# Kernel tuning notes

Hardware: AMD Instinct MI355X
Metric: run time of the kernel (lower is better)

Reference implementation:

```python
import jax, jax.numpy as jnp
from jax import lax
import numpy as np

B, T, F = 16, 1024, 128   # batch, time steps, freq bins (SPECTROGRAM_FRAME_LENGTH=1 -> frame feat = F = 128)
OUT = 61                  # phoneme classes
HID = 256


def _lengths_np():
    rng = np.random.default_rng(1)
    return rng.integers(T // 2, T + 1, size=B)


def conv2d(x, w, b, s):
    y = lax.conv_general_dilated(x, w, (s, s), 'VALID', dimension_numbers=('NCHW', 'OIHW', 'NCHW'))
    return y + b[None, :, None, None]


def bnorm(x, g, b, m, v):
    # eval-mode BatchNorm2d with running stats
    scale = g / jnp.sqrt(v + 1e-5)
    return (x - m[None, :, None, None]) * scale[None, :, None, None] + b[None, :, None, None]


def maxpool2(x):
    return lax.reduce_window(x, -np.inf, lax.max, (1, 1, 2, 2), (1, 1, 2, 2), 'VALID')


def resize_bilinear(x, h_src, H_out, W_out):
    # Bilinear resize (align_corners=False, no antialias), matching torchvision Resize on tensors.
    # x: [B,C,H,W]; per-sample valid height h_src (the crop r2[i,:,:h_i,:] is a prefix along H),
    # so gathering with indices < h_i is equivalent to resizing the cropped tensor. Vectorized over B.
    Bs, C, H, W = x.shape
    hs = h_src.astype(jnp.float32)
    c = (jnp.arange(H_out, dtype=jnp.float32)[None, :] + 0.5) * (hs[:, None] / H_out) - 0.5  # [B,H_out]
    c = jnp.maximum(c, 0.0)
    hi_max = h_src[:, None].astype(jnp.int32) - 1
    i0 = jnp.minimum(jnp.floor(c).astype(jnp.int32), hi_max)
    i1 = jnp.minimum(i0 + 1, hi_max)
    w1 = jnp.clip(c - i0.astype(jnp.float32), 0.0, 1.0)

    def gh(idx):
        return jnp.take_along_axis(x, jnp.broadcast_to(idx[:, None, :, None], (Bs, C, H_out, W)), axis=2)

    xh = gh(i0) * (1.0 - w1)[:, None, :, None] + gh(i1) * w1[:, None, :, None]  # [B,C,H_out,W]
    cw = (jnp.arange(W_out, dtype=jnp.float32) + 0.5) * (W / W_out) - 0.5
    cw = jnp.clip(cw, 0.0, W - 1.0)
    j0 = jnp.floor(cw).astype(jnp.int32)
    j1 = jnp.minimum(j0 + 1, W - 1)
    ww = cw - j0.astype(jnp.float32)
    return xh[..., j0] * (1.0 - ww) + xh[..., j1] * ww  # [B,C,H_out,W_out]


def gru_scan(x_tbd, wih, whh, bih, bhh):
    # PyTorch GRU cell, gate order (r, z, n). x_tbd: [T,B,D] -> [T,B,H]
    H = whh.shape[1]
    xW = jnp.einsum('tbd,gd->tbg', x_tbd, wih) + bih

    def step(h, xw):
        hW = h @ whh.T + bhh
        xr, xz, xn = jnp.split(xw, 3, -1)
        hr, hz, hn = jnp.split(hW, 3, -1)
        r = jax.nn.sigmoid(xr + hr)
        z = jax.nn.sigmoid(xz + hz)
        n = jnp.tanh(xn + r * hn)
        hnew = (1.0 - z) * n + z * h
        return hnew, hnew

    h0 = jnp.zeros((x_tbd.shape[1], H), x_tbd.dtype)
    return lax.scan(step, h0, xW)[1]


def bidir_gru(x, pf, pb, rev_idx):
    # x: [B,T,D]. rev_idx reverses only the valid prefix per sample (ragged lengths),
    # so the backward direction starts at each sample's true last frame, like per-sample torch GRU.
    of = gru_scan(x.transpose(1, 0, 2), *pf).transpose(1, 0, 2)
    xr = jnp.take_along_axis(x, rev_idx[:, :, None], axis=1)
    obr = gru_scan(xr.transpose(1, 0, 2), *pb).transpose(1, 0, 2)
    ob = jnp.take_along_axis(obr, rev_idx[:, :, None], axis=1)
    return jnp.concatenate([of, ob], -1)


def setup_inputs():
    keys = iter(jax.random.split(jax.random.key(0), 80))

    def rn(shape, s):
        return jax.random.normal(next(keys), shape, jnp.float32) * s

    d = {'batch': jax.random.normal(next(keys), (B, T, F), jnp.float32)}
    conv_defs = {'c1_4': (8, 1, 4), 'c1_8': (8, 1, 8), 'c1_16': (8, 1, 16), 'c1_32': (8, 1, 32),
                 'c2_4': (3, 8, 5), 'c2_8': (3, 8, 3), 'c2_16': (3, 8, 1), 'c2_32': (3, 8, 1)}
    for n, (o, i, k) in conv_defs.items():
        d[n + '_w'] = rn((o, i, k, k), 1.0 / np.sqrt(i * k * k))
        d[n + '_b'] = rn((o,), 0.05)
    for n, c in (('bn8', 8), ('bn3', 3)):
        d[n + '_g'] = 1.0 + rn((c,), 0.1)
        d[n + '_b'] = rn((c,), 0.1)
        d[n + '_m'] = rn((c,), 0.1)
        d[n + '_v'] = jax.random.uniform(next(keys), (c,), jnp.float32, 0.5, 1.5)
    d['fc1_w'] = rn((512, 5040), 0.02)
    d['fc1_b'] = rn((512,), 0.02)
    for l, din in ((0, 128 + 512), (1, 2 * HID)):
        for drc in 'fb':
            p = 'g%d%s_' % (l, drc)
            d[p + 'wih'] = rn((3 * HID, din), 1.0 / np.sqrt(HID))
            d[p + 'whh'] = rn((3 * HID, HID), 1.0 / np.sqrt(HID))
            d[p + 'bih'] = rn((3 * HID,), 0.05)
            d[p + 'bhh'] = rn((3 * HID,), 0.05)
    d['fc_w'] = rn((OUT, 2 * HID), 0.04)
    d['fc_b'] = rn((OUT,), 0.04)
    d['lengths'] = jnp.asarray(_lengths_np(), jnp.int32)
    return d


def reference(batch, c1_4_w, c1_4_b, c1_8_w, c1_8_b, c1_16_w, c1_16_b, c1_32_w, c1_32_b, c2_4_w, c2_4_b, c2_8_w, c2_8_b, c2_16_w, c2_16_b, c2_32_w, c2_32_b, bn8_g, bn8_b, bn8_m, bn8_v, bn3_g, bn3_b, bn3_m, bn3_v, fc1_w, fc1_b, g0f_wih, g0f_whh, g0f_bih, g0f_bhh, g0b_wih, g0b_whh, g0b_bih, g0b_bhh, g1f_wih, g1f_whh, g1f_bih, g1f_bhh, g1b_wih, g1b_whh, g1b_bih, g1b_bhh, fc_w, fc_b, lengths):
    Lnp = np.asarray(lengths)  # ragged lengths are static metadata
    max_len = float(Lnp.max())
    x = batch[:, None, :, :]
    # stage 1: multi-scale convs (shared bn8), relu, maxpool (dropout = identity in eval)
    r1_4 = maxpool2(jax.nn.relu(bnorm(conv2d(x, c1_4_w, c1_4_b, 1), bn8_g, bn8_b, bn8_m, bn8_v)))
    r1_8 = maxpool2(jax.nn.relu(bnorm(conv2d(x, c1_8_w, c1_8_b, 2), bn8_g, bn8_b, bn8_m, bn8_v)))
    r1_16 = maxpool2(jax.nn.relu(bnorm(conv2d(x, c1_16_w, c1_16_b, 4), bn8_g, bn8_b, bn8_m, bn8_v)))
    r1_32 = maxpool2(jax.nn.relu(bnorm(conv2d(x, c1_32_w, c1_32_b, 8), bn8_g, bn8_b, bn8_m, bn8_v)))
    # stage 2 (shared bn3)
    r2_4 = jax.nn.relu(bnorm(conv2d(r1_4, c2_4_w, c2_4_b, 3), bn3_g, bn3_b, bn3_m, bn3_v))
    r2_8 = jax.nn.relu(bnorm(conv2d(r1_8, c2_8_w, c2_8_b, 2), bn3_g, bn3_b, bn3_m, bn3_v))
    r2_16 = jax.nn.relu(bnorm(conv2d(r1_16, c2_16_w, c2_16_b, 1), bn3_g, bn3_b, bn3_m, bn3_v))
    r2_32 = jax.nn.relu(bnorm(conv2d(r1_32, c2_32_w, c2_32_b, 1), bn3_g, bn3_b, bn3_m, bn3_v))
    # per-sample crop (prefix in time) + resize to fixed sizes, fully batched
    feats = []
    for rr, (ho, wo) in ((r2_4, (90, 9)), (r2_8, (67, 6)), (r2_16, (67, 6)), (r2_32, (33, 2))):
        h_src = jnp.asarray((rr.shape[2] * (Lnp / max_len)).astype(np.int32))  # int() truncation
        feats.append(resize_bilinear(rr, h_src, ho, wo).reshape(B, -1))
    rfeat = jnp.concatenate(feats, axis=1) @ fc1_w.T + fc1_b  # [B,512]
    # frames (SPECTROGRAM_FRAME_LENGTH=1 -> frames == batch rows) + repeated global feature
    seq = jnp.concatenate([batch, jnp.broadcast_to(rfeat[:, None, :], (B, T, 512))], axis=-1)  # [B,T,640]
    tt = np.arange(T)[None, :]
    rev_idx = jnp.asarray(np.where(tt < Lnp[:, None], Lnp[:, None] - 1 - tt, tt).astype(np.int32))
    h = bidir_gru(seq, (g0f_wih, g0f_whh, g0f_bih, g0f_bhh), (g0b_wih, g0b_whh, g0b_bih, g0b_bhh), rev_idx)
    h = bidir_gru(h, (g1f_wih, g1f_whh, g1f_bih, g1f_bhh), (g1b_wih, g1b_whh, g1b_bih, g1b_bhh), rev_idx)
    preds = h @ fc_w.T + fc_b  # [B,T,OUT]
    rows = jnp.asarray(np.concatenate([i * T + np.arange(n) for i, n in enumerate(Lnp)]).astype(np.int32))
    return preds.reshape(B * T, OUT)[rows]  # [sum(lengths), OUT]
```

## Files before the change

kernel.cpp:

```cpp
#include <hip/hip_runtime.h>

typedef float f32;
typedef unsigned int u32;
typedef unsigned short u16;
typedef short s16x8 __attribute__((ext_vector_type(8)));
typedef float f32x4 __attribute__((ext_vector_type(4)));
typedef u32 u32x4 __attribute__((ext_vector_type(4)));

#define S1F (-1.4426950408889634f)
#define S2F ( 2.8853900817779268f)

__device__ __forceinline__ u16 f2bf(float x){
  u32 u = __float_as_uint(x);
  u32 r = u + 0x7FFFu + ((u >> 16) & 1u);
  return (u16)(r >> 16);
}

__global__ void k_meta(const int* __restrict__ lengths, int* __restrict__ meta){
  if (threadIdx.x == 0){
    int Lmax = 0;
    for (int b=0;b<16;b++) Lmax = max(Lmax, lengths[b]);
    meta[0] = Lmax;
    int acc = 0;
    for (int b=0;b<16;b++){ meta[1+b] = acc; acc += lengths[b]; }
    meta[17] = acc;
    const int H2s[4] = {169,126,126,62};
    for (int br=0;br<4;br++)
      for (int b=0;b<16;b++){
        double ratio = (double)lengths[b] / (double)Lmax;
        meta[32 + br*16 + b] = (int)((double)H2s[br] * ratio);
      }
  }
}

__global__ void k_wfrag(const f32* __restrict__ w0f, const f32* __restrict__ w0b,
                        const f32* __restrict__ w1f, const f32* __restrict__ w1b,
                        u16* __restrict__ wfrag){
  int idx = blockIdx.x*256 + threadIdx.x;
  int set = idx / 196608;
  int e   = idx % 196608;
  int w   = e / 24576;  int r  = e % 24576;
  int tau = r / 4096;   int r2 = r % 4096;
  int kc  = r2 >> 9;    int r3 = r2 & 511;
  int lane= r3 >> 3;    int j  = r3 & 7;
  int g = (tau>>1)*256 + w*32 + (tau&1)*16 + (lane & 15);
  int k = kc*32 + (lane>>4)*8 + j;
  const f32* src = (set==0)? w0f : (set==1)? w0b : (set==2)? w1f : w1b;
  float scale = (tau >= 4) ? S2F : S1F;
  wfrag[idx] = f2bf(src[g*256 + k] * scale);
}

__global__ void k_conv1(const f32* __restrict__ x, const f32* __restrict__ w, const f32* __restrict__ cb,
                        const f32* __restrict__ bg, const f32* __restrict__ bbp,
                        const f32* __restrict__ bm, const f32* __restrict__ bv,
                        f32* __restrict__ out, int K, int s, int Hp, int Wp){
  __shared__ f32 wl[8192];
  int b = blockIdx.y;
  int KK = K*K;
  for (int i=threadIdx.x; i<8*KK; i+=256) wl[i] = w[i];
  __syncthreads();
  int idx = blockIdx.x*256 + threadIdx.x;
  int npix = Hp*Wp;
  if (idx >= npix) return;
  int ph = idx / Wp, pw = idx % Wp;
  float mx[8];
  #pragma unroll
  for (int c=0;c<8;c++) mx[c] = -1e30f;
  for (int dy=0; dy<2; ++dy)
  for (int dx=0; dx<2; ++dx){
    const f32* xb = x + ((size_t)b*1024 + (size_t)(ph*2+dy)*s)*128 + (size_t)(pw*2+dx)*s;
    float acc[8];
    #pragma unroll
    for (int c=0;c<8;c++) acc[c] = 0.f;
    for (int kh=0; kh<K; ++kh){
      const f32* xr = xb + kh*128;
      for (int kw=0; kw<K; ++kw){
        float xv = xr[kw];
        #pragma unroll
        for (int c=0;c<8;c++) acc[c] = fmaf(xv, wl[c*KK + kh*K + kw], acc[c]);
      }
    }
    #pragma unroll
    for (int c=0;c<8;c++) mx[c] = fmaxf(mx[c], acc[c]);
  }
  #pragma unroll
  for (int c=0;c<8;c++){
    float scale = bg[c] * rsqrtf(bv[c] + 1e-5f);
    float val = (mx[c] + cb[c] - bm[c]) * scale + bbp[c];
    out[(((size_t)b*8 + c)*Hp + ph)*Wp + pw] = fmaxf(val, 0.f);
  }
}

__global__ void k_conv2(const f32* __restrict__ in, const f32* __restrict__ w, const f32* __restrict__ cb,
                        const f32* __restrict__ bg, const f32* __restrict__ bbp,
                        const f32* __restrict__ bm, const f32* __restrict__ bv,
                        f32* __restrict__ out, int K, int s, int Hin, int Win, int Ho, int Wo){
  __shared__ f32 wl[600];
  int b = blockIdx.y;
  int KK = K*K, sz = 24*KK;
  for (int i=threadIdx.x; i<sz; i+=256) wl[i] = w[i];
  __syncthreads();
  int idx = blockIdx.x*256 + threadIdx.x;
  int npix = Ho*Wo;
  if (idx >= npix) return;
  int oh = idx / Wo, ow = idx % Wo;
  float acc[3] = {0.f,0.f,0.f};
  for (int ci=0; ci<8; ++ci){
    const f32* xp = in + (((size_t)b*8 + ci)*Hin + (size_t)oh*s)*Win + (size_t)ow*s;
    for (int kh=0; kh<K; ++kh)
      for (int kw=0; kw<K; ++kw){
        float xv = xp[kh*Win + kw];
        #pragma unroll
        for (int co=0; co<3; ++co) acc[co] = fmaf(xv, wl[(co*8+ci)*KK + kh*K + kw], acc[co]);
      }
  }
  #pragma unroll
  for (int co=0; co<3; ++co){
    float scale = bg[co] * rsqrtf(bv[co] + 1e-5f);
    float val = (acc[co] + cb[co] - bm[co]) * scale + bbp[co];
    out[(((size_t)b*3 + co)*Ho + oh)*Wo + ow] = fmaxf(val, 0.f);
  }
}

__global__ void k_resize(const f32* __restrict__ src, const int* __restrict__ meta,
                         f32* __restrict__ feats, int H2, int W2, int Ho, int Wo, int off, int br){
  int idx = blockIdx.x*256 + threadIdx.x;
  int per_b = 3*Ho*Wo;
  if (idx >= 16*per_b) return;
  int b = idx / per_b;  int r = idx % per_b;
  int c = r / (Ho*Wo);  int r2 = r % (Ho*Wo);
  int ho = r2 / Wo, wo = r2 % Wo;
  int hs = meta[32 + br*16 + b];
  float cy = ((float)ho + 0.5f) * ((float)hs / (float)Ho) - 0.5f;
  cy = fmaxf(cy, 0.f);
  int him = hs - 1;
  int i0 = min((int)floorf(cy), him);
  int i1 = min(i0 + 1, him);
  float w1 = fminf(fmaxf(cy - (float)i0, 0.f), 1.f);
  float rw = (float)((double)W2 / (double)Wo);
  float cw = ((float)wo + 0.5f) * rw - 0.5f;
  cw = fminf(fmaxf(cw, 0.f), (float)(W2 - 1));
  int j0 = (int)floorf(cw);
  int j1 = min(j0 + 1, W2 - 1);
  float ww = cw - (float)j0;
  const f32* sp = src + (size_t)(b*3 + c) * H2 * W2;
  float v00 = sp[i0*W2 + j0], v01 = sp[i0*W2 + j1];
  float v10 = sp[i1*W2 + j0], v11 = sp[i1*W2 + j1];
  float col0 = v00*(1.f - w1) + v10*w1;
  float col1 = v01*(1.f - w1) + v11*w1;
  feats[(size_t)b*5040 + off + (c*Ho + ho)*Wo + wo] = col0*(1.f - ww) + col1*ww;
}

__global__ void k_fc1(const f32* __restrict__ feats, const f32* __restrict__ w,
                      const f32* __restrict__ bias, f32* __restrict__ rfeat){
  int b = blockIdx.x;
  int o0 = blockIdx.y * 64;
  int sub = threadIdx.x & 31, og = threadIdx.x >> 5;
  const f32* fp = feats + (size_t)b*5040;
  for (int oi = og; oi < 64; oi += 8){
    int o = o0 + oi;
    const f32* wp = w + (size_t)o*5040;
    float acc = 0.f;
    for (int k = sub; k < 5040; k += 32) acc = fmaf(fp[k], wp[k], acc);
    #pragma unroll
    for (int m=16; m; m>>=1) acc += __shfl_xor(acc, m, 32);
    if (sub == 0) rfeat[(size_t)b*512 + o] = acc + bias[o];
  }
}

__global__ void k_ydc(const f32* __restrict__ rfeat, const f32* __restrict__ wihf, const f32* __restrict__ wihb,
                      const f32* __restrict__ bihf, const f32* __restrict__ bihb, f32* __restrict__ ydc){
  int idx = blockIdx.x*256 + threadIdx.x;
  int d = idx / 12288;  int r = idx % 12288;
  int b = r / 768;      int g = r % 768;
  const f32* wih = d ? wihb : wihf;
  const f32* bih = d ? bihb : bihf;
  const f32* rp = rfeat + (size_t)b*512;
  const f32* wp = wih + (size_t)g*640 + 128;
  float acc = bih[g];
  for (int k=0;k<512;k++) acc = fmaf(rp[k], wp[k], acc);
  ydc[idx] = acc;
}

template<int LAYER>
__global__ __launch_bounds__(256)
void k_xw(const f32* __restrict__ A0, const f32* __restrict__ wihf, const f32* __restrict__ wihb,
          const f32* __restrict__ biasf, const f32* __restrict__ biasb,
          const f32* __restrict__ ydc, const f32* __restrict__ bhf, const f32* __restrict__ bhb,
          const int* __restrict__ lengths, f32* __restrict__ xwbuf){
  constexpr int KT   = (LAYER==0) ? 128 : 512;
  constexpr int WSTR = (LAYER==0) ? 640 : 512;
  int dir = blockIdx.z;
  const f32* wih = dir ? wihb : wihf;
  f32* out = xwbuf + (size_t)dir * 16384 * 768;
  int brow = blockIdx.x * 64, bcol = blockIdx.y * 64;
  __shared__ u32 As[1024], Bs[1024];
  int tid = threadIdx.x, lane = tid & 63, wid = tid >> 6;
  int rl = tid >> 2, kg = tid & 3;
  int grow = brow + rl;
  int tt = grow >> 4, bb = grow & 15;
  int srct = tt;
  if (dir){ int L = lengths[bb]; srct = (tt < L) ? (L - 1 - tt) : tt; }
  const f32* arow = A0 + ((size_t)bb*1024 + srct) * KT;
  const f32* brp  = wih + (size_t)(bcol + rl) * WSTR;
  int swst = kg ^ ((rl >> 1) & 3);
  u32* adst = &As[rl*16 + swst*4];
  u32* bdst = &Bs[rl*16 + swst*4];
  int r16 = wid*16 + (lane & 15);
  int grp = lane >> 4;
  int aoff = r16*16 + ((grp ^ ((r16 >> 1) & 3)) * 4);
  f32x4 acc[4];
  #pragma unroll
  for (int nt=0; nt<4; ++nt) acc[nt] = (f32x4){0.f,0.f,0.f,0.f};

  for (int kc=0; kc<KT/32; ++kc){
    int k0 = kc*32 + kg*8;
    {
      f32x4 av0 = *(const f32x4*)(arow + k0);
      f32x4 av1 = *(const f32x4*)(arow + k0 + 4);
      u32 p0 = (u32)f2bf(av0[0]) | ((u32)f2bf(av0[1])<<16);
      u32 p1 = (u32)f2bf(av0[2]) | ((u32)f2bf(av0[3])<<16);
      u32 p2 = (u32)f2bf(av1[0]) | ((u32)f2bf(av1[1])<<16);
      u32 p3 = (u32)f2bf(av1[2]) | ((u32)f2bf(av1[3])<<16);
      u32x4 v = {p0,p1,p2,p3};
      *(u32x4*)adst = v;
      f32x4 bv0 = *(const f32x4*)(brp + k0);
      f32x4 bv1 = *(const f32x4*)(brp + k0 + 4);
      u32 q0 = (u32)f2bf(bv0[0]) | ((u32)f2bf(bv0[1])<<16);
      u32 q1 = (u32)f2bf(bv0[2]) | ((u32)f2bf(bv0[3])<<16);
      u32 q2 = (u32)f2bf(bv1[0]) | ((u32)f2bf(bv1[1])<<16);
      u32 q3 = (u32)f2bf(bv1[2]) | ((u32)f2bf(bv1[3])<<16);
      u32x4 u = {q0,q1,q2,q3};
      *(u32x4*)bdst = u;
    }
    __syncthreads();
    s16x8 a = *(const s16x8*)&As[aoff];
    #pragma unroll
    for (int nt=0; nt<4; ++nt){
      int gl = nt*16 + (lane & 15);
      s16x8 bfr = *(const s16x8*)&Bs[gl*16 + ((grp ^ ((gl >> 1) & 3)) * 4)];
      acc[nt] = __builtin_amdgcn_mfma_f32_16x16x32_bf16(a, bfr, acc[nt], 0, 0, 0);
    }
    __syncthreads();
  }
  const f32* bh = dir ? bhb : bhf;
  #pragma unroll
  for (int nt=0; nt<4; ++nt){
    int col = bcol + nt*16 + (lane & 15);
    float bhadd = (col < 512) ? bh[col] : 0.f;
    float scale = (col < 512) ? S1F : S2F;
    #pragma unroll
    for (int q=0; q<4; ++q){
      int row = brow + wid*16 + (lane >> 4)*4 + q;
      float bias;
      if (LAYER == 0) bias = ydc[((size_t)dir*16 + (row & 15))*768 + col];
      else            bias = (dir ? biasb : biasf)[col];
      out[(size_t)row*768 + col] = (acc[nt][q] + bias + bhadd) * scale;
    }
  }
}

#define GRU_STEP(t_, u_, X_) do { \
  f32x4 a_r0={0.f,0.f,0.f,0.f}, a_r1={0.f,0.f,0.f,0.f}; \
  f32x4 a_z0={0.f,0.f,0.f,0.f}, a_z1={0.f,0.f,0.f,0.f}; \
  f32x4 a_n0={bhn0,bhn0,bhn0,bhn0}, a_n1={bhn1,bhn1,bhn1,bhn1}; \
  _Pragma("unroll") \
  for (int kc=0; kc<8; ++kc){ \
    s16x8 a = *(const s16x8*)&h_lds[(u_)*576 + hro + kc*32 + lq*8]; \
    a_r0 = __builtin_amdgcn_mfma_f32_16x16x32_bf16(a, wreg[0][kc], a_r0, 0,0,0); \
    a_r1 = __builtin_amdgcn_mfma_f32_16x16x32_bf16(a, wreg[1][kc], a_r1, 0,0,0); \
    a_z0 = __builtin_amdgcn_mfma_f32_16x16x32_bf16(a, wreg[2][kc], a_z0, 0,0,0); \
    a_z1 = __builtin_amdgcn_mfma_f32_16x16x32_bf16(a, wreg[3][kc], a_z1, 0,0,0); \
    a_n0 = __builtin_amdgcn_mfma_f32_16x16x32_bf16(a, wreg[4][kc], a_n0, 0,0,0); \
    a_n1 = __builtin_amdgcn_mfma_f32_16x16x32_bf16(a, wreg[5][kc], a_n1, 0,0,0); \
  } \
  { \
    float ar0 = qi ? a_r0[1] : a_r0[0], ar1 = qi ? a_r1[1] : a_r1[0]; \
    float az0 = qi ? a_z0[1] : a_z0[0], az1 = qi ? a_z1[1] : a_z1[0]; \
    float an0 = qi ? a_n0[1] : a_n0[0], an1 = qi ? a_n1[1] : a_n1[0]; \
    float ar = tpi ? ar1 : ar0; \
    float az = tpi ? az1 : az0; \
    float an = tpi ? an1 : an0; \
    float r = __builtin_amdgcn_rcpf(1.0f + __builtin_amdgcn_exp2f(X_[0] + ar)); \
    float z = __builtin_amdgcn_rcpf(1.0f + __builtin_amdgcn_exp2f(X_[1] + az)); \
    float n = fmaf(-2.0f, __builtin_amdgcn_rcpf(__builtin_amdgcn_exp2f(fmaf(r, an, X_[2])) + 1.0f), 1.0f); \
    float hv = fmaf(z, hp - n, n); \
    hp = hv; \
    u32 ub = __float_as_uint(hv); \
    h_lds[((u_)^1)*576 + qi*288 + jme] = (u16)((ub + 0x8000u)>>16); \
    if (dir == 0){ *hpt = hv; hpt += 512; } \
    else { int tpos = ((t_) < Lq) ? (Lq-1-(t_)) : (t_); hpt[(size_t)tpos*512] = hv; } \
  } \
  asm volatile("s_waitcnt lgkmcnt(0)\n\ts_barrier" ::: "memory"); \
} while(0)

template<int LAYER>
__global__ __launch_bounds__(512, 2)
void k_recur(const f32* __restrict__ xw, const u16* __restrict__ wfrag,
             const f32* __restrict__ bhhf, const f32* __restrict__ bhhb,
             const int* __restrict__ lengths, f32* __restrict__ hout){
  __shared__ u16 h_lds[1152];
  const int dir = blockIdx.y;
  const int b0  = blockIdx.x * 2;
  const int tid = threadIdx.x, lane = tid & 63, wid = tid >> 6;
  const f32* xwd = xw + (size_t)dir * 12582912;
  const f32* bhh = dir ? bhhb : bhhf;
  const u16* wf = wfrag + (size_t)(LAYER*2 + dir) * 196608;

  s16x8 wreg[6][8];
  #pragma unroll
  for (int tau=0; tau<6; ++tau)
    #pragma unroll
    for (int kc=0; kc<8; ++kc)
      wreg[tau][kc] = *(const s16x8*)(wf + ((size_t)((wid*6+tau)*8 + kc)*64 + lane)*8);
  if (tid < 576) ((u32*)h_lds)[tid] = 0;

  const int l15 = lane & 15, lq = lane >> 4;
  const int jlo = (wid << 5) + l15;
  const int hro = (l15 & 1) * 288;
  const int qi  = lq & 1;
  const int tpi = lq >> 1;
  const int jme = jlo + tpi*16;
  const float bhn0 = bhh[512 + jlo] * S2F;
  const float bhn1 = bhh[512 + jlo + 16] * S2F;
  const int Lq = lengths[b0 + qi];
  float hp = 0.f;

  const f32* xp = xwd + (size_t)(b0+qi)*768 + jme;
  f32* hpt = hout + (size_t)(b0+qi)*1024*512 + dir*256 + jme;

  float X0[3], X1[3];
  X0[0]=xp[0]; X0[1]=xp[256]; X0[2]=xp[512]; xp += 12288;
  X1[0]=xp[0]; X1[1]=xp[256]; X1[2]=xp[512]; xp += 12288;
  __syncthreads();

  for (int t2=0; t2<1024; t2+=2){
    GRU_STEP(t2,   0, X0);
    X0[0]=xp[0]; X0[1]=xp[256]; X0[2]=xp[512]; xp += 12288;
    GRU_STEP(t2+1, 1, X1);
    X1[0]=xp[0]; X1[1]=xp[256]; X1[2]=xp[512]; xp += 12288;
  }
}

__global__ void k_final(const f32* __restrict__ h1, const f32* __restrict__ fcw, const f32* __restrict__ fcb,
                        const int* __restrict__ lengths, const int* __restrict__ meta, f32* __restrict__ out){
  int t = blockIdx.x, b = blockIdx.y;
  if (t >= lengths[b]) return;
  __shared__ f32 part[4][64];
  int lane = threadIdx.x & 63, q = threadIdx.x >> 6;
  float acc = 0.f;
  if (lane < 61){
    const f32* wp = fcw + (size_t)lane*512 + q*128;
    const f32* hp = h1 + ((size_t)b*1024 + t)*512 + q*128;
    for (int k=0;k<128;k++) acc = fmaf(hp[k], wp[k], acc);
  }
  part[q][lane] = acc;
  __syncthreads();
  if (q == 0 && lane < 61){
    int row = meta[1 + b] + t;
    out[(size_t)row*61 + lane] = part[0][lane] + part[1][lane] + part[2][lane] + part[3][lane] + fcb[lane];
  }
}

extern "C" void kernel_launch(void* const* d_in, const int* in_sizes, int n_in,
                              void* d_out, int out_size, void* d_ws, size_t ws_size,
                              hipStream_t stream){
  const f32* batch = (const f32*)d_in[0];
  const f32* c1w[4] = {(const f32*)d_in[1],(const f32*)d_in[3],(const f32*)d_in[5],(const f32*)d_in[7]};
  const f32* c1b[4] = {(const f32*)d_in[2],(const f32*)d_in[4],(const f32*)d_in[6],(const f32*)d_in[8]};
  const f32* c2w[4] = {(const f32*)d_in[9],(const f32*)d_in[11],(const f32*)d_in[13],(const f32*)d_in[15]};
  const f32* c2b[4] = {(const f32*)d_in[10],(const f32*)d_in[12],(const f32*)d_in[14],(const f32*)d_in[16]};
  const f32 *bn8g=(const f32*)d_in[17], *bn8b=(const f32*)d_in[18], *bn8m=(const f32*)d_in[19], *bn8v=(const f32*)d_in[20];
  const f32 *bn3g=(const f32*)d_in[21], *bn3b=(const f32*)d_in[22], *bn3m=(const f32*)d_in[23], *bn3v=(const f32*)d_in[24];
  const f32 *fc1w=(const f32*)d_in[25], *fc1b=(const f32*)d_in[26];
  const f32 *g0f_wih=(const f32*)d_in[27], *g0f_whh=(const f32*)d_in[28], *g0f_bih=(const f32*)d_in[29], *g0f_bhh=(const f32*)d_in[30];
  const f32 *g0b_wih=(const f32*)d_in[31], *g0b_whh=(const f32*)d_in[32], *g0b_bih=(const f32*)d_in[33], *g0b_bhh=(const f32*)d_in[34];
  const f32 *g1f_wih=(const f32*)d_in[35], *g1f_whh=(const f32*)d_in[36], *g1f_bih=(const f32*)d_in[37], *g1f_bhh=(const f32*)d_in[38];
  const f32 *g1b_wih=(const f32*)d_in[39], *g1b_whh=(const f32*)d_in[40], *g1b_bih=(const f32*)d_in[41], *g1b_bhh=(const f32*)d_in[42];
  const f32 *fcw=(const f32*)d_in[43], *fcb=(const f32*)d_in[44];
  const int* lengths = (const int*)d_in[45];
  f32* out = (f32*)d_out;

  char* base = (char*)d_ws;
  size_t off = 0;
  auto alloc = [&](size_t bytes)->void*{
    void* p = base + off;
    off += bytes;
    off = (off + 255) & ~(size_t)255;
    return p;
  };

  static const int Hp[4]={510,254,126,62}, Wpp[4]={62,30,14,6};
  static const int K1[4]={4,8,16,32}, S1[4]={1,2,4,8};
  static const int K2[4]={5,3,1,1},  S2[4]={3,2,1,1};
  static const int Ho2[4]={169,126,126,62}, Wo2[4]={20,14,14,6};
  static const int Hr[4]={90,67,67,33}, Wr[4]={9,6,6,2};
  static const int Foff[4]={0,2430,3636,4842};

  f32* r1[4]; for (int i=0;i<4;i++) r1[i] = (f32*)alloc((size_t)16*8*Hp[i]*Wpp[i]*4);
  f32* r2[4]; for (int i=0;i<4;i++) r2[i] = (f32*)alloc((size_t)16*3*Ho2[i]*Wo2[i]*4);
  f32* feats = (f32*)alloc((size_t)16*5040*4);
  f32* rfeat = (f32*)alloc((size_t)16*512*4);
  f32* ydc   = (f32*)alloc((size_t)2*16*768*4);
  int* meta  = (int*)alloc(128*4);
  u16* wfrag = (u16*)alloc((size_t)4*196608*2);
  f32* xwb   = (f32*)alloc((size_t)2*1024*16*768*4);
  f32* h0    = (f32*)alloc((size_t)16*1024*512*4);
  f32* h1p   = (f32*)alloc((size_t)16*1024*512*4);

  k_meta<<<1,64,0,stream>>>(lengths, meta);
  k_wfrag<<<3072,256,0,stream>>>(g0f_whh, g0b_whh, g1f_whh, g1b_whh, wfrag);
  for (int i=0;i<4;i++){
    int np = Hp[i]*Wpp[i];
    k_conv1<<<dim3((np+255)/256,16),256,0,stream>>>(batch, c1w[i], c1b[i], bn8g,bn8b,bn8m,bn8v,
                                                    r1[i], K1[i], S1[i], Hp[i], Wpp[i]);
  }
  for (int i=0;i<4;i++){
    int np = Ho2[i]*Wo2[i];
    k_conv2<<<dim3((np+255)/256,16),256,0,stream>>>(r1[i], c2w[i], c2b[i], bn3g,bn3b,bn3m,bn3v,
                                                    r2[i], K2[i], S2[i], Hp[i], Wpp[i], Ho2[i], Wo2[i]);
  }
  for (int i=0;i<4;i++){
    int tot = 16*3*Hr[i]*Wr[i];
    k_resize<<<(tot+255)/256,256,0,stream>>>(r2[i], meta, feats, Ho2[i], Wo2[i], Hr[i], Wr[i], Foff[i], i);
  }
  k_fc1<<<dim3(16,8),256,0,stream>>>(feats, fc1w, fc1b, rfeat);
  k_ydc<<<96,256,0,stream>>>(rfeat, g0f_wih, g0b_wih, g0f_bih, g0b_bih, ydc);
  k_xw<0><<<dim3(256,12,2),256,0,stream>>>(batch, g0f_wih, g0b_wih, nullptr, nullptr, ydc, g0f_bhh, g0b_bhh, lengths, xwb);
  k_recur<0><<<dim3(8,2),512,0,stream>>>(xwb, wfrag, g0f_bhh, g0b_bhh, lengths, h0);
  k_xw<1><<<dim3(256,12,2),256,0,stream>>>(h0, g1f_wih, g1b_wih, g1f_bih, g1b_bih, nullptr, g1f_bhh, g1b_bhh, lengths, xwb);
  k_recur<1><<<dim3(8,2),512,0,stream>>>(xwb, wfrag, g1f_bhh, g1b_bhh, lengths, h1p);
  k_final<<<dim3(1024,16),256,0,stream>>>(h1p, fcw, fcb, lengths, meta, out);
}
```

Baseline: 2.914 ms.

## Store hidden states in bf16, pre-convert GEMM operands, merge branch launches

Several changes at once. Input and Wih weights are converted to bf16 once in a merged prep kernel, and k_xw loads them straight into LDS with global_load_lds instead of converting in the loop. The recurrence now writes bf16 hidden states, which halves the h buffer traffic. The per-branch conv and resize launches are merged into single grid-z kernels, and k_final is restructured to process 16 timesteps per block with vectorized loads. The extra bf16 rounding of h now also feeds the final FC, which may slightly change numerics.

```diff
diff --git a/kernel.cpp b/kernel.cpp
--- a/kernel.cpp
+++ b/kernel.cpp
@@ -16,8 +16,48 @@
   return (u16)(r >> 16);
 }
 
-__global__ void k_meta(const int* __restrict__ lengths, int* __restrict__ meta){
-  if (threadIdx.x == 0){
+__device__ __forceinline__ void gld16(const u16* g, u16* l){
+  __builtin_amdgcn_global_load_lds((const __attribute__((address_space(1))) u32*)g,
+                                   (__attribute__((address_space(3))) u32*)l, 16, 0, 0);
+}
+
+__global__ void k_prep(const f32* __restrict__ w0f, const f32* __restrict__ w0b,
+                       const f32* __restrict__ w1f, const f32* __restrict__ w1b,
+                       const f32* __restrict__ wih0f, const f32* __restrict__ wih0b,
+                       const f32* __restrict__ wih1f, const f32* __restrict__ wih1b,
+                       const f32* __restrict__ batch, const int* __restrict__ lengths,
+                       u16* __restrict__ wfrag, u16* __restrict__ wihbf,
+                       u16* __restrict__ batchbf, int* __restrict__ meta){
+  const int bx = blockIdx.x, tid = threadIdx.x;
+  if (bx < 3072){
+    int idx = bx*256 + tid;
+    int set = idx / 196608;
+    int e   = idx % 196608;
+    int w   = e / 24576;  int r  = e % 24576;
+    int tau = r / 4096;   int r2 = r % 4096;
+    int kc  = r2 >> 9;    int r3 = r2 & 511;
+    int lane= r3 >> 3;    int j  = r3 & 7;
+    int g = (tau>>1)*256 + w*32 + (tau&1)*16 + (lane & 15);
+    int k = kc*32 + (lane>>4)*8 + j;
+    const f32* src = (set==0)? w0f : (set==1)? w0b : (set==2)? w1f : w1b;
+    float scale = (tau >= 4) ? S2F : S1F;
+    wfrag[idx] = f2bf(src[g*256 + k] * scale);
+  } else if (bx < 6912){
+    int idx = (bx-3072)*256 + tid;
+    if (idx < 196608){
+      int d = idx / 98304; int r = idx % 98304;
+      int g = r >> 7, k = r & 127;
+      wihbf[idx] = f2bf((d ? wih0b : wih0f)[g*640 + k]);
+    } else {
+      int i2 = idx - 196608;
+      int d = i2 / 393216; int r = i2 % 393216;
+      int g = r >> 9, k = r & 511;
+      wihbf[idx] = f2bf((d ? wih1b : wih1f)[g*512 + k]);
+    }
+  } else if (bx < 15104){
+    int idx = (bx-6912)*256 + tid;
+    batchbf[idx] = f2bf(batch[idx]);
+  } else if (tid == 0){
     int Lmax = 0;
     for (int b=0;b<16;b++) Lmax = max(Lmax, lengths[b]);
     meta[0] = Lmax;
@@ -33,27 +73,18 @@
   }
 }
 
-__global__ void k_wfrag(const f32* __restrict__ w0f, const f32* __restrict__ w0b,
-                        const f32* __restrict__ w1f, const f32* __restrict__ w1b,
-                        u16* __restrict__ wfrag){
-  int idx = blockIdx.x*256 + threadIdx.x;
-  int set = idx / 196608;
-  int e   = idx % 196608;
-  int w   = e / 24576;  int r  = e % 24576;
-  int tau = r / 4096;   int r2 = r % 4096;
-  int kc  = r2 >> 9;    int r3 = r2 & 511;
-  int lane= r3 >> 3;    int j  = r3 & 7;
-  int g = (tau>>1)*256 + w*32 + (tau&1)*16 + (lane & 15);
-  int k = kc*32 + (lane>>4)*8 + j;
-  const f32* src = (set==0)? w0f : (set==1)? w0b : (set==2)? w1f : w1b;
-  float scale = (tau >= 4) ? S2F : S1F;
-  wfrag[idx] = f2bf(src[g*256 + k] * scale);
-}
-
-__global__ void k_conv1(const f32* __restrict__ x, const f32* __restrict__ w, const f32* __restrict__ cb,
-                        const f32* __restrict__ bg, const f32* __restrict__ bbp,
-                        const f32* __restrict__ bm, const f32* __restrict__ bv,
-                        f32* __restrict__ out, int K, int s, int Hp, int Wp){
+__global__ void k_conv1a(const f32* __restrict__ x,
+                         const f32* __restrict__ w0,const f32* __restrict__ w1,const f32* __restrict__ w2,const f32* __restrict__ w3,
+                         const f32* __restrict__ cb0,const f32* __restrict__ cb1,const f32* __restrict__ cb2,const f32* __restrict__ cb3,
+                         const f32* __restrict__ bg, const f32* __restrict__ bbp,
+                         const f32* __restrict__ bm, const f32* __restrict__ bv,
+                         f32* __restrict__ o0, f32* __restrict__ o1, f32* __restrict__ o2, f32* __restrict__ o3){
+  const int br = blockIdx.z;
+  const int Ks[4]={4,8,16,32}, Ss[4]={1,2,4,8}, Hps[4]={510,254,126,62}, Wps[4]={62,30,14,6};
+  const int K = Ks[br], s = Ss[br], Hp = Hps[br], Wp = Wps[br];
+  const f32* w  = (br==0)?w0:(br==1)?w1:(br==2)?w2:w3;
+  const f32* cb = (br==0)?cb0:(br==1)?cb1:(br==2)?cb2:cb3;
+  f32* out      = (br==0)?o0:(br==1)?o1:(br==2)?o2:o3;
   __shared__ f32 wl[8192];
   int b = blockIdx.y;
   int KK = K*K;
@@ -91,10 +122,20 @@
   }
 }
 
-__global__ void k_conv2(const f32* __restrict__ in, const f32* __restrict__ w, const f32* __restrict__ cb,
-                        const f32* __restrict__ bg, const f32* __restrict__ bbp,
-                        const f32* __restrict__ bm, const f32* __restrict__ bv,
-                        f32* __restrict__ out, int K, int s, int Hin, int Win, int Ho, int Wo){
+__global__ void k_conv2a(const f32* __restrict__ i0,const f32* __restrict__ i1,const f32* __restrict__ i2,const f32* __restrict__ i3,
+                         const f32* __restrict__ w0,const f32* __restrict__ w1,const f32* __restrict__ w2,const f32* __restrict__ w3,
+                         const f32* __restrict__ cb0,const f32* __restrict__ cb1,const f32* __restrict__ cb2,const f32* __restrict__ cb3,
+                         const f32* __restrict__ bg, const f32* __restrict__ bbp,
+                         const f32* __restrict__ bm, const f32* __restrict__ bv,
+                         f32* __restrict__ o0, f32* __restrict__ o1, f32* __restrict__ o2, f32* __restrict__ o3){
+  const int br = blockIdx.z;
+  const int Ks[4]={5,3,1,1}, Ss[4]={3,2,1,1}, Hins[4]={510,254,126,62}, Wins[4]={62,30,14,6};
+  const int Hos[4]={169,126,126,62}, Wos[4]={20,14,14,6};
+  const int K = Ks[br], s = Ss[br], Hin = Hins[br], Win = Wins[br], Ho = Hos[br], Wo = Wos[br];
+  const f32* in = (br==0)?i0:(br==1)?i1:(br==2)?i2:i3;
+  const f32* w  = (br==0)?w0:(br==1)?w1:(br==2)?w2:w3;
+  const f32* cb = (br==0)?cb0:(br==1)?cb1:(br==2)?cb2:cb3;
+  f32* out      = (br==0)?o0:(br==1)?o1:(br==2)?o2:o3;
   __shared__ f32 wl[600];
   int b = blockIdx.y;
   int KK = K*K, sz = 24*KK;
@@ -122,8 +163,13 @@
   }
 }
 
-__global__ void k_resize(const f32* __restrict__ src, const int* __restrict__ meta,
-                         f32* __restrict__ feats, int H2, int W2, int Ho, int Wo, int off, int br){
+__global__ void k_resizea(const f32* __restrict__ s0,const f32* __restrict__ s1,const f32* __restrict__ s2,const f32* __restrict__ s3,
+                          const int* __restrict__ meta, f32* __restrict__ feats){
+  const int br = blockIdx.z;
+  const int H2s[4]={169,126,126,62}, W2s[4]={20,14,14,6}, Hos[4]={90,67,67,33}, Wos[4]={9,6,6,2};
+  const int offs[4]={0,2430,3636,4842};
+  const int H2 = H2s[br], W2 = W2s[br], Ho = Hos[br], Wo = Wos[br], off = offs[br];
+  const f32* src = (br==0)?s0:(br==1)?s1:(br==2)?s2:s3;
   int idx = blockIdx.x*256 + threadIdx.x;
   int per_b = 3*Ho*Wo;
   if (idx >= 16*per_b) return;
@@ -175,70 +221,55 @@
   int b = r / 768;      int g = r % 768;
   const f32* wih = d ? wihb : wihf;
   const f32* bih = d ? bihb : bihf;
-  const f32* rp = rfeat + (size_t)b*512;
-  const f32* wp = wih + (size_t)g*640 + 128;
+  const f32x4* rp = (const f32x4*)(rfeat + (size_t)b*512);
+  const f32x4* wp = (const f32x4*)(wih + (size_t)g*640 + 128);
   float acc = bih[g];
-  for (int k=0;k<512;k++) acc = fmaf(rp[k], wp[k], acc);
+  for (int k=0;k<128;k++){
+    f32x4 a = rp[k], w4 = wp[k];
+    acc = fmaf(a[0],w4[0],acc); acc = fmaf(a[1],w4[1],acc);
+    acc = fmaf(a[2],w4[2],acc); acc = fmaf(a[3],w4[3],acc);
+  }
   ydc[idx] = acc;
 }
 
 template<int LAYER>
 __global__ __launch_bounds__(256)
-void k_xw(const f32* __restrict__ A0, const f32* __restrict__ wihf, const f32* __restrict__ wihb,
+void k_xw(const u16* __restrict__ Abf, const u16* __restrict__ wihbf,
           const f32* __restrict__ biasf, const f32* __restrict__ biasb,
           const f32* __restrict__ ydc, const f32* __restrict__ bhf, const f32* __restrict__ bhb,
           const int* __restrict__ lengths, f32* __restrict__ xwbuf){
-  constexpr int KT   = (LAYER==0) ? 128 : 512;
-  constexpr int WSTR = (LAYER==0) ? 640 : 512;
-  int dir = blockIdx.z;
-  const f32* wih = dir ? wihb : wihf;
+  constexpr int KT = (LAYER==0) ? 128 : 512;
+  const int dir = blockIdx.z;
   f32* out = xwbuf + (size_t)dir * 16384 * 768;
-  int brow = blockIdx.x * 64, bcol = blockIdx.y * 64;
-  __shared__ u32 As[1024], Bs[1024];
-  int tid = threadIdx.x, lane = tid & 63, wid = tid >> 6;
-  int rl = tid >> 2, kg = tid & 3;
-  int grow = brow + rl;
-  int tt = grow >> 4, bb = grow & 15;
+  const u16* wd = wihbf + (size_t)dir * 768 * KT;
+  const int brow = blockIdx.x * 64, bcol = blockIdx.y * 64;
+  __shared__ __attribute__((aligned(16))) u16 As[2048], Bs[2048];
+  const int tid = threadIdx.x, lane = tid & 63, wid = tid >> 6;
+  const int srow = wid*16 + (lane >> 2);
+  const int cg   = (lane & 3) ^ (srow & 3);
+  int tt = (brow + srow) >> 4, bb = (brow + srow) & 15;
   int srct = tt;
   if (dir){ int L = lengths[bb]; srct = (tt < L) ? (L - 1 - tt) : tt; }
-  const f32* arow = A0 + ((size_t)bb*1024 + srct) * KT;
-  const f32* brp  = wih + (size_t)(bcol + rl) * WSTR;
-  int swst = kg ^ ((rl >> 1) & 3);
-  u32* adst = &As[rl*16 + swst*4];
-  u32* bdst = &Bs[rl*16 + swst*4];
-  int r16 = wid*16 + (lane & 15);
-  int grp = lane >> 4;
-  int aoff = r16*16 + ((grp ^ ((r16 >> 1) & 3)) * 4);
+  const u16* asrc = Abf + ((size_t)bb*1024 + srct)*KT + cg*8;
+  const u16* bsrc = wd + (size_t)(bcol + srow)*KT + cg*8;
+  u16* adst = As + wid*512;
+  u16* bdst = Bs + wid*512;
+  const int l15 = lane & 15, grp = lane >> 4;
+  const int arow_f = wid*16 + l15;
+  const int aoff = arow_f*32 + ((grp ^ (arow_f & 3))*8);
   f32x4 acc[4];
   #pragma unroll
   for (int nt=0; nt<4; ++nt) acc[nt] = (f32x4){0.f,0.f,0.f,0.f};
 
   for (int kc=0; kc<KT/32; ++kc){
-    int k0 = kc*32 + kg*8;
-    {
-      f32x4 av0 = *(const f32x4*)(arow + k0);
-      f32x4 av1 = *(const f32x4*)(arow + k0 + 4);
-      u32 p0 = (u32)f2bf(av0[0]) | ((u32)f2bf(av0[1])<<16);
-      u32 p1 = (u32)f2bf(av0[2]) | ((u32)f2bf(av0[3])<<16);
-      u32 p2 = (u32)f2bf(av1[0]) | ((u32)f2bf(av1[1])<<16);
-      u32 p3 = (u32)f2bf(av1[2]) | ((u32)f2bf(av1[3])<<16);
-      u32x4 v = {p0,p1,p2,p3};
-      *(u32x4*)adst = v;
-      f32x4 bv0 = *(const f32x4*)(brp + k0);
-      f32x4 bv1 = *(const f32x4*)(brp + k0 + 4);
-      u32 q0 = (u32)f2bf(bv0[0]) | ((u32)f2bf(bv0[1])<<16);
-      u32 q1 = (u32)f2bf(bv0[2]) | ((u32)f2bf(bv0[3])<<16);
-      u32 q2 = (u32)f2bf(bv1[0]) | ((u32)f2bf(bv1[1])<<16);
-      u32 q3 = (u32)f2bf(bv1[2]) | ((u32)f2bf(bv1[3])<<16);
-      u32x4 u = {q0,q1,q2,q3};
-      *(u32x4*)bdst = u;
-    }
+    gld16(asrc + kc*32, adst);
+    gld16(bsrc + kc*32, bdst);
     __syncthreads();
     s16x8 a = *(const s16x8*)&As[aoff];
     #pragma unroll
     for (int nt=0; nt<4; ++nt){
-      int gl = nt*16 + (lane & 15);
-      s16x8 bfr = *(const s16x8*)&Bs[gl*16 + ((grp ^ ((gl >> 1) & 3)) * 4)];
+      int cb = nt*16 + l15;
+      s16x8 bfr = *(const s16x8*)&Bs[cb*32 + ((grp ^ (cb & 3))*8)];
       acc[nt] = __builtin_amdgcn_mfma_f32_16x16x32_bf16(a, bfr, acc[nt], 0, 0, 0);
     }
     __syncthreads();
@@ -246,12 +277,12 @@
   const f32* bh = dir ? bhb : bhf;
   #pragma unroll
   for (int nt=0; nt<4; ++nt){
-    int col = bcol + nt*16 + (lane & 15);
+    int col = bcol + nt*16 + l15;
     float bhadd = (col < 512) ? bh[col] : 0.f;
     float scale = (col < 512) ? S1F : S2F;
     #pragma unroll
     for (int q=0; q<4; ++q){
-      int row = brow + wid*16 + (lane >> 4)*4 + q;
+      int row = brow + wid*16 + grp*4 + q;
       float bias;
       if (LAYER == 0) bias = ydc[((size_t)dir*16 + (row & 15))*768 + col];
       else            bias = (dir ? biasb : biasf)[col];
@@ -287,9 +318,10 @@
     float hv = fmaf(z, hp - n, n); \
     hp = hv; \
     u32 ub = __float_as_uint(hv); \
-    h_lds[((u_)^1)*576 + qi*288 + jme] = (u16)((ub + 0x8000u)>>16); \
-    if (dir == 0){ *hpt = hv; hpt += 512; } \
-    else { int tpos = ((t_) < Lq) ? (Lq-1-(t_)) : (t_); hpt[(size_t)tpos*512] = hv; } \
+    u16 hb16 = (u16)((ub + 0x8000u)>>16); \
+    h_lds[((u_)^1)*576 + qi*288 + jme] = hb16; \
+    if (dir == 0){ *hb = hb16; hb += 512; } \
+    else { int tpos = ((t_) < Lq) ? (Lq-1-(t_)) : (t_); hb[(size_t)tpos*512] = hb16; } \
   } \
   asm volatile("s_waitcnt lgkmcnt(0)\n\ts_barrier" ::: "memory"); \
 } while(0)
@@ -298,7 +330,7 @@
 __global__ __launch_bounds__(512, 2)
 void k_recur(const f32* __restrict__ xw, const u16* __restrict__ wfrag,
              const f32* __restrict__ bhhf, const f32* __restrict__ bhhb,
-             const int* __restrict__ lengths, f32* __restrict__ hout){
+             const int* __restrict__ lengths, u16* __restrict__ hbf){
   __shared__ u16 h_lds[1152];
   const int dir = blockIdx.y;
   const int b0  = blockIdx.x * 2;
@@ -327,7 +359,7 @@
   float hp = 0.f;
 
   const f32* xp = xwd + (size_t)(b0+qi)*768 + jme;
-  f32* hpt = hout + (size_t)(b0+qi)*1024*512 + dir*256 + jme;
+  u16* hb = hbf + ((size_t)(b0+qi)*1024)*512 + dir*256 + jme;
 
   float X0[3], X1[3];
   X0[0]=xp[0]; X0[1]=xp[256]; X0[2]=xp[512]; xp += 12288;
@@ -342,23 +374,37 @@
   }
 }
 
-__global__ void k_final(const f32* __restrict__ h1, const f32* __restrict__ fcw, const f32* __restrict__ fcb,
+__global__ void k_final(const u16* __restrict__ h1, const f32* __restrict__ fcw, const f32* __restrict__ fcb,
                         const int* __restrict__ lengths, const int* __restrict__ meta, f32* __restrict__ out){
-  int t = blockIdx.x, b = blockIdx.y;
-  if (t >= lengths[b]) return;
-  __shared__ f32 part[4][64];
-  int lane = threadIdx.x & 63, q = threadIdx.x >> 6;
-  float acc = 0.f;
-  if (lane < 61){
-    const f32* wp = fcw + (size_t)lane*512 + q*128;
-    const f32* hp = h1 + ((size_t)b*1024 + t)*512 + q*128;
-    for (int k=0;k<128;k++) acc = fmaf(hp[k], wp[k], acc);
-  }
-  part[q][lane] = acc;
-  __syncthreads();
-  if (q == 0 && lane < 61){
-    int row = meta[1 + b] + t;
-    out[(size_t)row*61 + lane] = part[0][lane] + part[1][lane] + part[2][lane] + part[3][lane] + fcb[lane];
+  int b = blockIdx.y;
+  int t0 = blockIdx.x * 16;
+  int lane = threadIdx.x & 63, w = threadIdx.x >> 6;
+  int L = lengths[b];
+  if (t0 >= L) return;
+  const f32* wp = fcw + (size_t)lane*512;
+  float bias = (lane < 61) ? fcb[lane] : 0.f;
+  int rowbase = meta[1 + b];
+  #pragma unroll
+  for (int p=0;p<4;p++){
+    int t = t0 + p*4 + w;
+    if (t < L && lane < 61){
+      const u16* hp = h1 + ((size_t)b*1024 + t)*512;
+      float acc = 0.f;
+      for (int k8=0;k8<64;k8++){
+        u32x4 hv = *(const u32x4*)(hp + k8*8);
+        f32x4 w0 = *(const f32x4*)(wp + k8*8);
+        f32x4 w1 = *(const f32x4*)(wp + k8*8 + 4);
+        acc = fmaf(__uint_as_float(hv[0] << 16),        w0[0], acc);
+        acc = fmaf(__uint_as_float(hv[0] & 0xffff0000u),w0[1], acc);
+        acc = fmaf(__uint_as_float(hv[1] << 16),        w0[2], acc);
+        acc = fmaf(__uint_as_float(hv[1] & 0xffff0000u),w0[3], acc);
+        acc = fmaf(__uint_as_float(hv[2] << 16),        w1[0], acc);
+        acc = fmaf(__uint_as_float(hv[2] & 0xffff0000u),w1[1], acc);
+        acc = fmaf(__uint_as_float(hv[3] << 16),        w1[2], acc);
+        acc = fmaf(__uint_as_float(hv[3] & 0xffff0000u),w1[3], acc);
+      }
+      out[(size_t)(rowbase + t)*61 + lane] = acc + bias;
+    }
   }
 }
 
@@ -391,11 +437,7 @@
   };
 
   static const int Hp[4]={510,254,126,62}, Wpp[4]={62,30,14,6};
-  static const int K1[4]={4,8,16,32}, S1[4]={1,2,4,8};
-  static const int K2[4]={5,3,1,1},  S2[4]={3,2,1,1};
   static const int Ho2[4]={169,126,126,62}, Wo2[4]={20,14,14,6};
-  static const int Hr[4]={90,67,67,33}, Wr[4]={9,6,6,2};
-  static const int Foff[4]={0,2430,3636,4842};
 
   f32* r1[4]; for (int i=0;i<4;i++) r1[i] = (f32*)alloc((size_t)16*8*Hp[i]*Wpp[i]*4);
   f32* r2[4]; for (int i=0;i<4;i++) r2[i] = (f32*)alloc((size_t)16*3*Ho2[i]*Wo2[i]*4);
@@ -404,31 +446,30 @@
   f32* ydc   = (f32*)alloc((size_t)2*16*768*4);
   int* meta  = (int*)alloc(128*4);
   u16* wfrag = (u16*)alloc((size_t)4*196608*2);
+  u16* wihbf = (u16*)alloc((size_t)983040*2);
+  u16* batchbf=(u16*)alloc((size_t)16*1024*128*2);
   f32* xwb   = (f32*)alloc((size_t)2*1024*16*768*4);
-  f32* h0    = (f32*)alloc((size_t)16*1024*512*4);
-  f32* h1p   = (f32*)alloc((size_t)16*1024*512*4);
-
-  k_meta<<<1,64,0,stream>>>(lengths, meta);
-  k_wfrag<<<3072,256,0,stream>>>(g0f_whh, g0b_whh, g1f_whh, g1b_whh, wfrag);
-  for (int i=0;i<4;i++){
-    int np = Hp[i]*Wpp[i];
-    k_conv1<<<dim3((np+255)/256,16),256,0,stream>>>(batch, c1w[i], c1b[i], bn8g,bn8b,bn8m,bn8v,
-                                                    r1[i], K1[i], S1[i], Hp[i], Wpp[i]);
-  }
-  for (int i=0;i<4;i++){
-    int np = Ho2[i]*Wo2[i];
-    k_conv2<<<dim3((np+255)/256,16),256,0,stream>>>(r1[i], c2w[i], c2b[i], bn3g,bn3b,bn3m,bn3v,
-                                                    r2[i], K2[i], S2[i], Hp[i], Wpp[i], Ho2[i], Wo2[i]);
-  }
-  for (int i=0;i<4;i++){
-    int tot = 16*3*Hr[i]*Wr[i];
-    k_resize<<<(tot+255)/256,256,0,stream>>>(r2[i], meta, feats, Ho2[i], Wo2[i], Hr[i], Wr[i], Foff[i], i);
-  }
+  u16* hbf0  = (u16*)alloc((size_t)16*1024*512*2);
+  u16* hbf1  = (u16*)alloc((size_t)16*1024*512*2);
+
+  k_prep<<<15105,256,0,stream>>>(g0f_whh, g0b_whh, g1f_whh, g1b_whh,
+                                 g0f_wih, g0b_wih, g1f_wih, g1b_wih,
+                                 batch, lengths, wfrag, wihbf, batchbf, meta);
+  k_conv1a<<<dim3(124,16,4),256,0,stream>>>(batch, c1w[0],c1w[1],c1w[2],c1w[3],
+                                            c1b[0],c1b[1],c1b[2],c1b[3],
+                                            bn8g,bn8b,bn8m,bn8v, r1[0],r1[1],r1[2],r1[3]);
+  k_conv2a<<<dim3(14,16,4),256,0,stream>>>(r1[0],r1[1],r1[2],r1[3],
+                                           c2w[0],c2w[1],c2w[2],c2w[3],
+                                           c2b[0],c2b[1],c2b[2],c2b[3],
+                                           bn3g,bn3b,bn3m,bn3v, r2[0],r2[1],r2[2],r2[3]);
+  k_resizea<<<dim3(152,1,4),256,0,stream>>>(r2[0],r2[1],r2[2],r2[3], meta, feats);
   k_fc1<<<dim3(16,8),256,0,stream>>>(feats, fc1w, fc1b, rfeat);
   k_ydc<<<96,256,0,stream>>>(rfeat, g0f_wih, g0b_wih, g0f_bih, g0b_bih, ydc);
-  k_xw<0><<<dim3(256,12,2),256,0,stream>>>(batch, g0f_wih, g0b_wih, nullptr, nullptr, ydc, g0f_bhh, g0b_bhh, lengths, xwb);
-  k_recur<0><<<dim3(8,2),512,0,stream>>>(xwb, wfrag, g0f_bhh, g0b_bhh, lengths, h0);
-  k_xw<1><<<dim3(256,12,2),256,0,stream>>>(h0, g1f_wih, g1b_wih, g1f_bih, g1b_bih, nullptr, g1f_bhh, g1b_bhh, lengths, xwb);
-  k_recur<1><<<dim3(8,2),512,0,stream>>>(xwb, wfrag, g1f_bhh, g1b_bhh, lengths, h1p);
-  k_final<<<dim3(1024,16),256,0,stream>>>(h1p, fcw, fcb, lengths, meta, out);
-}
+  k_xw<0><<<dim3(256,12,2),256,0,stream>>>(batchbf, wihbf, nullptr, nullptr,
+                                           ydc, g0f_bhh, g0b_bhh, lengths, xwb);
+  k_recur<0><<<dim3(8,2),512,0,stream>>>(xwb, wfrag, g0f_bhh, g0b_bhh, lengths, hbf0);
+  k_xw<1><<<dim3(256,12,2),256,0,stream>>>(hbf0, wihbf + 196608, g1f_bih, g1b_bih,
+                                           nullptr, g1f_bhh, g1b_bhh, lengths, xwb);
+  k_recur<1><<<dim3(8,2),512,0,stream>>>(xwb, wfrag, g1f_bhh, g1b_bhh, lengths, hbf1);
+  k_final<<<dim3(64,16),256,0,stream>>>(hbf1, fcw, fcb, lengths, meta, out);
+}
```

Result: no change. 2.930 ms, median of 2 (+0.5%).
